# Kernel tuning notes

Measured on AMD Instinct MI355X. Metric: run time of the kernel, lower is better.

## Reference

```python
import jax, jax.numpy as jnp
import numpy as np

B, T, OBS, E, H, A = 256, 128, 512, 1024, 1024, 64


def setup_inputs() -> dict:
    key = jax.random.key(0)
    ks = jax.random.split(key, 8)
    s = 0.02
    return {
        "obs": jax.random.normal(ks[0], (B, T, OBS), jnp.float32),
        "h0": jnp.zeros((B, H), jnp.float32),
        "c0": jnp.zeros((B, H), jnp.float32),
        "W1": jax.random.normal(ks[1], (OBS, E), jnp.float32) * s,
        "b1": jnp.zeros((E,), jnp.float32),
        "W2": jax.random.normal(ks[2], (E, E), jnp.float32) * s,
        "b2": jnp.zeros((E,), jnp.float32),
        "w_ih": jax.random.normal(ks[3], (4 * H, E), jnp.float32) * s,
        "w_hh": jax.random.normal(ks[4], (4 * H, H), jnp.float32) * s,
        "b_ih": jnp.zeros((4 * H,), jnp.float32).at[H:2 * H].set(1.0),  # forget-gate bias init
        "b_hh": jnp.zeros((4 * H,), jnp.float32),
        "ln_g": jnp.ones((H,), jnp.float32),
        "ln_b": jnp.zeros((H,), jnp.float32),
        "Wa": jax.random.normal(ks[5], (H, A), jnp.float32) * s,
        "ba": jnp.zeros((A,), jnp.float32),
        "Wc": jax.random.normal(ks[6], (H, 1), jnp.float32) * s,
        "bc": jnp.zeros((1,), jnp.float32),
        "Wobs": jax.random.normal(ks[7], (H, OBS), jnp.float32) * s,
        "bobs": jnp.zeros((OBS,), jnp.float32),
        "Wr": jax.random.normal(jax.random.fold_in(key, 9), (H, 1), jnp.float32) * s,
        "br": jnp.zeros((1,), jnp.float32),
    }


def _layernorm(x, g, b, eps=1e-5):
    mu = jnp.mean(x, axis=-1, keepdims=True)
    var = jnp.mean(jnp.square(x - mu), axis=-1, keepdims=True)
    return (x - mu) * jax.lax.rsqrt(var + eps) * g + b


def reference(obs, h0, c0, W1, b1, W2, b2, w_ih, w_hh, b_ih, b_hh,
              ln_g, ln_b, Wa, ba, Wc, bc, Wobs, bobs, Wr, br):
    # obs encoder: Linear -> SiLU -> Linear -> SiLU   [B,T,OBS] -> [B,T,E]
    enc = jax.nn.silu(jax.nn.silu(obs @ W1 + b1) @ W2 + b2)
    # precompute input contribution to gates (batched GEMM): [B,T,4H]
    gx = jnp.einsum('bte,ge->btg', enc, w_ih) + (b_ih + b_hh)
    gx_t = jnp.transpose(gx, (1, 0, 2))  # [T,B,4H] for scan

    Hs = h0.shape[-1]

    def step(carry, g_in):
        h, c = carry
        gates = g_in + h @ w_hh.T  # [B,4H]
        i = jax.nn.sigmoid(gates[:, :Hs])
        f = jax.nn.sigmoid(gates[:, Hs:2 * Hs])
        g = jnp.tanh(gates[:, 2 * Hs:3 * Hs])
        o = jax.nn.sigmoid(gates[:, 3 * Hs:])
        new_c = f * c + i * g
        new_h = o * jnp.tanh(new_c)
        return (new_h, new_c), new_h

    (hT, cT), h_seq = jax.lax.scan(step, (h0, c0), gx_t)  # h_seq: [T,B,H]
    h_seq = jnp.transpose(h_seq, (1, 0, 2))  # [B,T,H] batch-first internal format

    x = _layernorm(h_seq, ln_g, ln_b)
    logits = x @ Wa + ba            # [B,T,A]
    values = x @ Wc + bc            # [B,T,1]
    obs_pred = x @ Wobs + bobs      # [B,T,OBS]
    rew_pred = x @ Wr + br          # [B,T,1]
    return (logits, values, obs_pred, rew_pred, hT, cT)
```

## Files before the change

kernel.cpp:

```cpp
#include <hip/hip_runtime.h>
#include <cstdint>

constexpr int Bb = 256, Tt = 128, OBSn = 512, Ee = 1024, Hh = 1024, Aa = 64;
constexpr int Tc = 16;

typedef __attribute__((ext_vector_type(8))) short bf16x8;
typedef __attribute__((ext_vector_type(4))) float floatx4;

__device__ __forceinline__ unsigned short f2bf(float f) {
  union { float f; unsigned u; } c; c.f = f;
  unsigned r = c.u + 0x7fffu + ((c.u >> 16) & 1u);
  return (unsigned short)(r >> 16);
}
__device__ __forceinline__ float bf2f(unsigned short h) {
  union { unsigned u; float f; } c; c.u = ((unsigned)h) << 16; return c.f;
}
__device__ __forceinline__ void gload16(const void* g, void* l) {
  __builtin_amdgcn_global_load_lds(
      (__attribute__((address_space(1))) void*)(uintptr_t)g,
      (__attribute__((address_space(3))) void*)l, 16, 0, 0);
}
__device__ __forceinline__ float sigmoidf_(float x) { return 1.f / (1.f + __expf(-x)); }
__device__ __forceinline__ float tanhf_(float x) { return 2.f / (1.f + __expf(-2.f * x)) - 1.f; }

template <int EPI>
__global__ __launch_bounds__(512) void gemm256(
    const unsigned short* __restrict__ A, const unsigned short* __restrict__ Bt,
    const float* __restrict__ bias, void* __restrict__ Cout,
    int M, int N, int K, int ldo) {
  __shared__ __align__(16) unsigned short sm[4][256 * 64];
  const int tid = threadIdx.x;
  const int wave = tid >> 6, lane = tid & 63;
  const int quad = lane >> 4, l16 = lane & 15;
  const int nwg = gridDim.x;
  const int wg = (blockIdx.x & 7) * (nwg >> 3) + (blockIdx.x >> 3);
  const int nbn = N >> 8;
  const int m0 = (wg / nbn) * 256, n0 = (wg % nbn) * 256;
  const int wm = (wave >> 2) * 128, wn = (wave & 3) * 64;

  floatx4 zero = {0.f, 0.f, 0.f, 0.f};
  floatx4 acc[8][4];
#pragma unroll
  for (int i = 0; i < 8; ++i)
#pragma unroll
    for (int j = 0; j < 4; ++j) acc[i][j] = zero;

  const int nk = K >> 6;
  auto stage = [&](int p, int k0) {
#pragma unroll
    for (int s = 0; s < 4; ++s) {
      const int c = s * 512 + tid;
      const int row = c >> 3;
      const int sl = (c & 7) ^ (row & 7);
      const int lb = (s * 512 + wave * 64) * 8;
      gload16(A + (size_t)(m0 + row) * K + k0 + sl * 8, &sm[p][lb]);
      gload16(Bt + (size_t)(n0 + row) * K + k0 + sl * 8, &sm[2 + p][lb]);
    }
  };
  stage(0, 0);
  stage(1, 1 << 6);
  for (int kt = 0; kt < nk; ++kt) {
    if (kt + 1 < nk) asm volatile("s_waitcnt vmcnt(8)" ::: "memory");
    else             asm volatile("s_waitcnt vmcnt(0)" ::: "memory");
    __builtin_amdgcn_s_barrier();
    const int p = kt & 1;
#pragma unroll
    for (int kk = 0; kk < 2; ++kk) {
      bf16x8 af[8], bfr[4];
#pragma unroll
      for (int i = 0; i < 8; ++i) {
        const int row = wm + i * 16 + l16;
        af[i] = *(const bf16x8*)&sm[p][row * 64 + (((kk * 4 + quad) ^ (l16 & 7)) << 3)];
      }
#pragma unroll
      for (int j = 0; j < 4; ++j) {
        const int row = wn + j * 16 + l16;
        bfr[j] = *(const bf16x8*)&sm[2 + p][row * 64 + (((kk * 4 + quad) ^ (l16 & 7)) << 3)];
      }
#pragma unroll
      for (int i = 0; i < 8; ++i)
#pragma unroll
        for (int j = 0; j < 4; ++j)
          acc[i][j] = __builtin_amdgcn_mfma_f32_16x16x32_bf16(af[i], bfr[j], acc[i][j], 0, 0, 0);
    }
    __builtin_amdgcn_s_barrier();
    if (kt + 2 < nk) stage(p, (kt + 2) << 6);
  }

  if (EPI == 3) {
#pragma unroll
    for (int i = 0; i < 8; ++i)
#pragma unroll
      for (int j = 0; j < 4; ++j) {
        const int col = n0 + wn + j * 16 + l16;
        const float bv = bias[col];
#pragma unroll
        for (int r = 0; r < 4; ++r) {
          const int row = m0 + wm + i * 16 + quad * 4 + r;
          ((float*)Cout)[(size_t)row * ldo + col] = acc[i][j][r] + bv;
        }
      }
  } else {
    __syncthreads();
    unsigned short* Cs = &sm[0][0];
#pragma unroll
    for (int i = 0; i < 8; ++i)
#pragma unroll
      for (int j = 0; j < 4; ++j) {
        const int coll = wn + j * 16 + l16;
        float bv = 0.f;
        if (EPI == 0 || EPI == 1) bv = bias[n0 + coll];
#pragma unroll
        for (int r = 0; r < 4; ++r) {
          const int rowl = wm + i * 16 + quad * 4 + r;
          float v = acc[i][j][r];
          if (EPI == 0 || EPI == 1) {
            v += bv;
            v = v * sigmoidf_(v);
          }
          Cs[rowl * 256 + (coll ^ (quad << 4))] = f2bf(v);
        }
      }
    __syncthreads();
#pragma unroll
    for (int pp = 0; pp < 16; ++pp) {
      const int c2 = pp * 4096 + tid * 8;
      const int rowl = c2 >> 8, coll = c2 & 255;
      const bf16x8 val = *(const bf16x8*)&Cs[rowl * 256 + (coll ^ (((rowl >> 2) & 3) << 4))];
      size_t orow;
      if (EPI == 1) {
        const int grow = m0 + rowl;
        orow = (size_t)((grow & (Tt - 1)) * Bb + (grow >> 7));
      } else {
        orow = (size_t)(m0 + rowl);
      }
      *(bf16x8*)((unsigned short*)Cout + orow * ldo + n0 + coll) = val;
    }
  }
}

template <int EPI>
__global__ __launch_bounds__(256) void gemm_bt(
    const unsigned short* __restrict__ A, const unsigned short* __restrict__ Bt,
    const float* __restrict__ bias, void* __restrict__ Cout,
    int M, int N, int K, int ldo, int nreal) {
  __shared__ __align__(16) unsigned short sm[4][128 * 32];
  const int tid = threadIdx.x;
  const int wave = tid >> 6, lane = tid & 63;
  const int quad = lane >> 4, l16 = lane & 15;
  const int m0 = blockIdx.x * 128, n0 = blockIdx.y * 128;
  const int wm = (wave >> 1) * 64, wn = (wave & 1) * 64;

  floatx4 zero = {0.f, 0.f, 0.f, 0.f};
  floatx4 acc[4][4];
#pragma unroll
  for (int i = 0; i < 4; ++i)
#pragma unroll
    for (int j = 0; j < 4; ++j) acc[i][j] = zero;

  const int nk = K >> 5;
  auto stage = [&](int p, int k0) {
#pragma unroll
    for (int r = 0; r < 2; ++r) {
      const int cb = (r * 4 + wave) * 64;
      const int c = cb + lane;
      const int row = c >> 2, kp = (c & 3) << 3;
      gload16(A + (size_t)(m0 + row) * K + k0 + kp, &sm[p][cb * 8]);
      gload16(Bt + (size_t)(n0 + row) * K + k0 + kp, &sm[2 + p][cb * 8]);
    }
  };
  stage(0, 0);
  for (int kt = 0; kt < nk; ++kt) {
    __syncthreads();
    if (kt + 1 < nk) stage((kt + 1) & 1, (kt + 1) << 5);
    const int p = kt & 1;
    bf16x8 af[4], bfr[4];
#pragma unroll
    for (int i = 0; i < 4; ++i)
      af[i] = *(const bf16x8*)&sm[p][(wm + i * 16 + l16) * 32 + quad * 8];
#pragma unroll
    for (int i = 0; i < 4; ++i)
      bfr[i] = *(const bf16x8*)&sm[2 + p][(wn + i * 16 + l16) * 32 + quad * 8];
#pragma unroll
    for (int i = 0; i < 4; ++i)
#pragma unroll
      for (int j = 0; j < 4; ++j)
        acc[i][j] = __builtin_amdgcn_mfma_f32_16x16x32_bf16(af[i], bfr[j], acc[i][j], 0, 0, 0);
  }
#pragma unroll
  for (int i = 0; i < 4; ++i) {
#pragma unroll
    for (int j = 0; j < 4; ++j) {
      const int col = n0 + wn + j * 16 + l16;
#pragma unroll
      for (int r = 0; r < 4; ++r) {
        const int row = m0 + wm + i * 16 + quad * 4 + r;
        float v = acc[i][j][r];
        if (col < nreal) {
          v += bias[col];
          ((float*)Cout)[(size_t)row * ldo + col] = v;
        }
      }
    }
  }
}

__global__ __launch_bounds__(256) void lstm_step(
    const unsigned short* __restrict__ hprev, long long hstride,
    const unsigned short* __restrict__ whh,
    const unsigned short* __restrict__ gxt,
    const float* __restrict__ bias4h,
    float* __restrict__ c_st, float* __restrict__ hTf,
    unsigned short* __restrict__ hseq_t,
    int write_hT) {
  __shared__ __align__(16) unsigned short As[2][4][64 * 32];
  __shared__ __align__(16) unsigned short Bs[2][4][64 * 32];
  const int bid = blockIdx.x;
  const int xcd = bid & 7, slot = bid >> 3;
  const int m0 = (slot & 3) * 64;
  const int nh0 = (xcd + ((slot >> 2) << 3)) * 16;
  const int tid = threadIdx.x;
  const int wave = tid >> 6, lane = tid & 63;
  const int quad = lane >> 4, l16 = lane & 15;

  floatx4 zero = {0.f, 0.f, 0.f, 0.f};
  floatx4 acc[4] = {zero, zero, zero, zero};

  const int row = tid >> 2, kp = (tid & 3) << 3;
  const int wrow = ((row >> 4) << 10) + nh0 + (row & 15);
  const unsigned short* asrc = hprev + (size_t)(m0 + row) * hstride + kp;
  const unsigned short* bsrc = whh + (size_t)wrow * Hh + kp;

  auto stage = [&](int p, int k0) {
#pragma unroll
    for (int s = 0; s < 4; ++s) {
      gload16(asrc + k0 + s * 32, &As[p][s][wave * 512]);
      gload16(bsrc + k0 + s * 32, &Bs[p][s][wave * 512]);
    }
  };
  stage(0, 0);
  stage(1, 128);
  for (int kt = 0; kt < 8; ++kt) {
    if (kt + 1 < 8) asm volatile("s_waitcnt vmcnt(8)" ::: "memory");
    else            asm volatile("s_waitcnt vmcnt(0)" ::: "memory");
    __builtin_amdgcn_s_barrier();
    const int p = kt & 1;
#pragma unroll
    for (int s = 0; s < 4; ++s) {
      bf16x8 af = *(const bf16x8*)&As[p][s][(wave * 16 + l16) * 32 + quad * 8];
#pragma unroll
      for (int g = 0; g < 4; ++g) {
        bf16x8 bfr = *(const bf16x8*)&Bs[p][s][(g * 16 + l16) * 32 + quad * 8];
        acc[g] = __builtin_amdgcn_mfma_f32_16x16x32_bf16(af, bfr, acc[g], 0, 0, 0);
      }
    }
    __builtin_amdgcn_s_barrier();
    if (kt + 2 < 8) stage(p, (kt + 2) << 7);
  }
  const int col = nh0 + l16;
#pragma unroll
  for (int r = 0; r < 4; ++r) {
    const int b = m0 + wave * 16 + quad * 4 + r;
    float pre[4];
#pragma unroll
    for (int g = 0; g < 4; ++g)
      pre[g] = acc[g][r] + bf2f(gxt[(size_t)b * 4096 + (g << 10) + col]) + bias4h[(g << 10) + col];
    const float ig = sigmoidf_(pre[0]);
    const float fg = sigmoidf_(pre[1]);
    const float gg = tanhf_(pre[2]);
    const float og = sigmoidf_(pre[3]);
    const size_t idx = (size_t)b * Hh + col;
    const float cn = fg * c_st[idx] + ig * gg;
    c_st[idx] = cn;
    const float hn = og * tanhf_(cn);
    if (write_hT) hTf[idx] = hn;
    hseq_t[(size_t)b * (Tt * Hh) + col] = f2bf(hn);
  }
}

__global__ __launch_bounds__(256) void ln_head(
    const unsigned short* __restrict__ hseq, const float* __restrict__ g,
    const float* __restrict__ b, const float* __restrict__ Wc, const float* __restrict__ bc,
    const float* __restrict__ Wr, const float* __restrict__ br,
    unsigned short* __restrict__ xout, float* __restrict__ vout, float* __restrict__ rout) {
  const int row = blockIdx.x;
  const int tid = threadIdx.x;
  const int wave = tid >> 6, lane = tid & 63;
  __shared__ float red[4][4];
  const ushort4 hv = ((const ushort4*)(hseq + (size_t)row * Hh))[tid];
  float h[4] = {bf2f(hv.x), bf2f(hv.y), bf2f(hv.z), bf2f(hv.w)};
  float s = h[0] + h[1] + h[2] + h[3];
  float ss = h[0] * h[0] + h[1] * h[1] + h[2] * h[2] + h[3] * h[3];
#pragma unroll
  for (int o = 32; o > 0; o >>= 1) { s += __shfl_xor(s, o); ss += __shfl_xor(ss, o); }
  if (lane == 0) { red[0][wave] = s; red[1][wave] = ss; }
  __syncthreads();
  s = red[0][0] + red[0][1] + red[0][2] + red[0][3];
  ss = red[1][0] + red[1][1] + red[1][2] + red[1][3];
  const float mu = s * (1.f / 1024.f);
  const float var = ss * (1.f / 1024.f) - mu * mu;
  const float rs = rsqrtf(var + 1e-5f);
  const float4 gv = ((const float4*)g)[tid];
  const float4 bv = ((const float4*)b)[tid];
  const float4 wcv = ((const float4*)Wc)[tid];
  const float4 wrv = ((const float4*)Wr)[tid];
  const float x0 = (h[0] - mu) * rs * gv.x + bv.x;
  const float x1 = (h[1] - mu) * rs * gv.y + bv.y;
  const float x2 = (h[2] - mu) * rs * gv.z + bv.z;
  const float x3 = (h[3] - mu) * rs * gv.w + bv.w;
  ushort4 pk; pk.x = f2bf(x0); pk.y = f2bf(x1); pk.z = f2bf(x2); pk.w = f2bf(x3);
  ((ushort4*)(xout + (size_t)row * Hh))[tid] = pk;
  float v = x0 * wcv.x + x1 * wcv.y + x2 * wcv.z + x3 * wcv.w;
  float r = x0 * wrv.x + x1 * wrv.y + x2 * wrv.z + x3 * wrv.w;
#pragma unroll
  for (int o = 32; o > 0; o >>= 1) { v += __shfl_xor(v, o); r += __shfl_xor(r, o); }
  if (lane == 0) { red[2][wave] = v; red[3][wave] = r; }
  __syncthreads();
  if (tid == 0) {
    vout[row] = red[2][0] + red[2][1] + red[2][2] + red[2][3] + bc[0];
    rout[row] = red[3][0] + red[3][1] + red[3][2] + red[3][3] + br[0];
  }
}

__global__ __launch_bounds__(256) void cvt_bf16x4(const float4* __restrict__ in,
                                                  ushort4* __restrict__ out, int n4) {
  const int i = blockIdx.x * 256 + threadIdx.x;
  if (i < n4) {
    const float4 v = in[i];
    ushort4 o; o.x = f2bf(v.x); o.y = f2bf(v.y); o.z = f2bf(v.z); o.w = f2bf(v.w);
    out[i] = o;
  }
}
__global__ __launch_bounds__(256) void transpose_cvt(const float* __restrict__ in,
                                                     unsigned short* __restrict__ out,
                                                     int K, int N, int NPAD) {
  __shared__ float tile[32][33];
  const int tx = threadIdx.x & 31, ty = threadIdx.x >> 5;
  const int k0 = blockIdx.x * 32, n0 = blockIdx.y * 32;
#pragma unroll
  for (int i = 0; i < 32; i += 8) {
    const int k = k0 + ty + i, n = n0 + tx;
    tile[ty + i][tx] = (n < N && k < K) ? in[(size_t)k * N + n] : 0.f;
  }
  __syncthreads();
#pragma unroll
  for (int i = 0; i < 32; i += 8) {
    const int n = n0 + ty + i, k = k0 + tx;
    if (n < NPAD && k < K) out[(size_t)n * K + k] = f2bf(tile[tx][ty + i]);
  }
}
__global__ __launch_bounds__(256) void prep_kernel(
    const float* __restrict__ b_ih, const float* __restrict__ b_hh, float* __restrict__ bias4h,
    const float* __restrict__ h0, const float* __restrict__ c0,
    unsigned short* __restrict__ h0bf, float* __restrict__ c_st) {
  const int i = blockIdx.x * 256 + threadIdx.x;
  if (i < 4096) bias4h[i] = b_ih[i] + b_hh[i];
  h0bf[i] = f2bf(h0[i]);
  c_st[i] = c0[i];
}
__global__ __launch_bounds__(256) void copy_hc(const float* __restrict__ h,
                                               const float* __restrict__ c,
                                               float* __restrict__ oh, float* __restrict__ oc) {
  const int i = blockIdx.x * 256 + threadIdx.x;
  oh[i] = h[i];
  oc[i] = c[i];
}

constexpr size_t SZ_W1T = (size_t)Ee * OBSn * 2;
constexpr size_t SZ_W2T = (size_t)Ee * Ee * 2;
constexpr size_t SZ_WAT = (size_t)128 * Hh * 2;
constexpr size_t SZ_WOBST = (size_t)OBSn * Hh * 2;
constexpr size_t SZ_WIH = (size_t)4 * Hh * Ee * 2;
constexpr size_t SZ_WHH = (size_t)4 * Hh * Hh * 2;
constexpr size_t SZ_BIAS = 4096 * 4;
constexpr size_t SZ_H0BF = (size_t)Bb * Hh * 2;
constexpr size_t SZ_CST = (size_t)Bb * Hh * 4;
constexpr size_t SZ_HTF = (size_t)Bb * Hh * 4;
constexpr size_t SZ_R1 = (size_t)Bb * Tt * OBSn * 2;
constexpr size_t SZ_R2 = (size_t)Bb * Tt * Ee * 2;

constexpr size_t OFF_W1T = 0;
constexpr size_t OFF_W2T = OFF_W1T + SZ_W1T;
constexpr size_t OFF_WAT = OFF_W2T + SZ_W2T;
constexpr size_t OFF_WOBST = OFF_WAT + SZ_WAT;
constexpr size_t OFF_WIH = OFF_WOBST + SZ_WOBST;
constexpr size_t OFF_WHH = OFF_WIH + SZ_WIH;
constexpr size_t OFF_BIAS = OFF_WHH + SZ_WHH;
constexpr size_t OFF_H0BF = OFF_BIAS + SZ_BIAS;
constexpr size_t OFF_CST = OFF_H0BF + SZ_H0BF;
constexpr size_t OFF_HTF = OFF_CST + SZ_CST;
constexpr size_t OFF_R1 = OFF_HTF + SZ_HTF;
constexpr size_t OFF_R2 = OFF_R1 + SZ_R1;
constexpr size_t WS_NEED = OFF_R2 + SZ_R2;

constexpr size_t OFF_LOGITS = 0;
constexpr size_t OFF_V = (size_t)Bb * Tt * Aa;
constexpr size_t OFF_OBS = OFF_V + (size_t)Bb * Tt;
constexpr size_t OFF_R = OFF_OBS + (size_t)Bb * Tt * OBSn;
constexpr size_t OFF_HT = OFF_R + (size_t)Bb * Tt;
constexpr size_t OFF_CT = OFF_HT + (size_t)Bb * Hh;

extern "C" void kernel_launch(void* const* d_in, const int* in_sizes, int n_in,
                              void* d_out, int out_size, void* d_ws, size_t ws_size,
                              hipStream_t stream) {
  if (ws_size < WS_NEED) return;

  const float* obs = (const float*)d_in[0];
  const float* h0 = (const float*)d_in[1];
  const float* c0 = (const float*)d_in[2];
  const float* W1 = (const float*)d_in[3];
  const float* b1 = (const float*)d_in[4];
  const float* W2 = (const float*)d_in[5];
  const float* b2 = (const float*)d_in[6];
  const float* w_ih = (const float*)d_in[7];
  const float* w_hh = (const float*)d_in[8];
  const float* b_ih = (const float*)d_in[9];
  const float* b_hh = (const float*)d_in[10];
  const float* ln_g = (const float*)d_in[11];
  const float* ln_b = (const float*)d_in[12];
  const float* Wa = (const float*)d_in[13];
  const float* ba = (const float*)d_in[14];
  const float* Wc = (const float*)d_in[15];
  const float* bc = (const float*)d_in[16];
  const float* Wobs = (const float*)d_in[17];
  const float* bobs = (const float*)d_in[18];
  const float* Wr = (const float*)d_in[19];
  const float* br = (const float*)d_in[20];

  char* ws = (char*)d_ws;
  unsigned short* w1t = (unsigned short*)(ws + OFF_W1T);
  unsigned short* w2t = (unsigned short*)(ws + OFF_W2T);
  unsigned short* wat = (unsigned short*)(ws + OFF_WAT);
  unsigned short* wobst = (unsigned short*)(ws + OFF_WOBST);
  unsigned short* wih = (unsigned short*)(ws + OFF_WIH);
  unsigned short* whh = (unsigned short*)(ws + OFF_WHH);
  float* bias4h = (float*)(ws + OFF_BIAS);
  unsigned short* h0bf = (unsigned short*)(ws + OFF_H0BF);
  float* cst = (float*)(ws + OFF_CST);
  float* htf = (float*)(ws + OFF_HTF);
  unsigned short* obsbf = (unsigned short*)(ws + OFF_R1);
  unsigned short* gxc = (unsigned short*)(ws + OFF_R1);
  unsigned short* enc2t = (unsigned short*)(ws + OFF_R2);
  unsigned short* xbuf = (unsigned short*)(ws + OFF_R2);
  float* out = (float*)d_out;
  unsigned short* enc1 = (unsigned short*)(out + OFF_OBS);
  unsigned short* hseq = (unsigned short*)(out + OFF_OBS);

  const dim3 blk(256);
  const dim3 blk512(512);

  prep_kernel<<<dim3(1024), blk, 0, stream>>>(b_ih, b_hh, bias4h, h0, c0, h0bf, cst);
  cvt_bf16x4<<<dim3(16384), blk, 0, stream>>>((const float4*)obs, (ushort4*)obsbf, 4194304);
  cvt_bf16x4<<<dim3(4096), blk, 0, stream>>>((const float4*)w_ih, (ushort4*)wih, 1048576);
  cvt_bf16x4<<<dim3(4096), blk, 0, stream>>>((const float4*)w_hh, (ushort4*)whh, 1048576);
  transpose_cvt<<<dim3(16, 32), blk, 0, stream>>>(W1, w1t, OBSn, Ee, Ee);
  transpose_cvt<<<dim3(32, 32), blk, 0, stream>>>(W2, w2t, Ee, Ee, Ee);
  transpose_cvt<<<dim3(32, 4), blk, 0, stream>>>(Wa, wat, Hh, Aa, 128);
  transpose_cvt<<<dim3(32, 16), blk, 0, stream>>>(Wobs, wobst, Hh, OBSn, OBSn);

  gemm256<0><<<dim3(512), blk512, 0, stream>>>(obsbf, w1t, b1, enc1, 32768, Ee, OBSn, Ee);
  gemm256<1><<<dim3(512), blk512, 0, stream>>>(enc1, w2t, b2, enc2t, 32768, Ee, Ee, Ee);

  for (int ch = 0; ch < Tt / Tc; ++ch) {
    gemm256<2><<<dim3(256), blk512, 0, stream>>>(enc2t + (size_t)ch * Tc * Bb * Ee, wih, nullptr,
                                                 gxc, Tc * Bb, 4096, Ee, 4096);
    for (int l = 0; l < Tc; ++l) {
      const int t = ch * Tc + l;
      const unsigned short* hp = (t == 0) ? h0bf : hseq + (size_t)(t - 1) * Hh;
      const long long hs = (t == 0) ? (long long)Hh : (long long)Tt * Hh;
      lstm_step<<<dim3(256), blk, 0, stream>>>(hp, hs, whh, gxc + (size_t)l * Bb * 4096,
                                               bias4h, cst, htf, hseq + (size_t)t * Hh,
                                               (t == Tt - 1) ? 1 : 0);
    }
  }

  ln_head<<<dim3(32768), blk, 0, stream>>>(hseq, ln_g, ln_b, Wc, bc, Wr, br, xbuf,
                                           out + OFF_V, out + OFF_R);
  gemm_bt<3><<<dim3(256, 1), blk, 0, stream>>>(xbuf, wat, ba, out + OFF_LOGITS, 32768, 128, Hh, Aa, Aa);
  gemm256<3><<<dim3(256), blk512, 0, stream>>>(xbuf, wobst, bobs, out + OFF_OBS, 32768, OBSn, Hh, OBSn);
  copy_hc<<<dim3(1024), blk, 0, stream>>>(htf, cst, out + OFF_HT, out + OFF_CT);

  (void)in_sizes; (void)n_in; (void)out_size;
}
```

Before: 2.031 ms.

## Interleave GEMM tile prefetch chunks with MFMA quarter-steps and raise wave priority

```diff
diff --git a/kernel.cpp b/kernel.cpp
--- a/kernel.cpp
+++ b/kernel.cpp
@@ -22,6 +22,11 @@
 }
 __device__ __forceinline__ float sigmoidf_(float x) { return 1.f / (1.f + __expf(-x)); }
 __device__ __forceinline__ float tanhf_(float x) { return 2.f / (1.f + __expf(-2.f * x)) - 1.f; }
+
+template <int N> __device__ __forceinline__ void waitv() {
+  if constexpr (N == 0) asm volatile("s_waitcnt vmcnt(0)" ::: "memory");
+  else asm volatile("s_waitcnt vmcnt(2)" ::: "memory");
+}
 
 template <int EPI>
 __global__ __launch_bounds__(512) void gemm256(
@@ -46,45 +51,58 @@
     for (int j = 0; j < 4; ++j) acc[i][j] = zero;
 
   const int nk = K >> 6;
-  auto stage = [&](int p, int k0) {
-#pragma unroll
-    for (int s = 0; s < 4; ++s) {
-      const int c = s * 512 + tid;
-      const int row = c >> 3;
-      const int sl = (c & 7) ^ (row & 7);
-      const int lb = (s * 512 + wave * 64) * 8;
-      gload16(A + (size_t)(m0 + row) * K + k0 + sl * 8, &sm[p][lb]);
-      gload16(Bt + (size_t)(n0 + row) * K + k0 + sl * 8, &sm[2 + p][lb]);
-    }
+  auto sub = [&](const unsigned short* G, int gb, int r0, int k0, unsigned short* dst) {
+    const int row = r0 + (tid >> 3);
+    const int sl = (tid & 7) ^ (row & 7);
+    gload16(G + (size_t)(gb + row) * K + k0 + sl * 8, dst + (size_t)(r0 * 8 + wave * 64) * 8);
   };
-  stage(0, 0);
-  stage(1, 1 << 6);
-  for (int kt = 0; kt < nk; ++kt) {
-    if (kt + 1 < nk) asm volatile("s_waitcnt vmcnt(8)" ::: "memory");
-    else             asm volatile("s_waitcnt vmcnt(0)" ::: "memory");
-    __builtin_amdgcn_s_barrier();
-    const int p = kt & 1;
-#pragma unroll
-    for (int kk = 0; kk < 2; ++kk) {
-      bf16x8 af[8], bfr[4];
-#pragma unroll
-      for (int i = 0; i < 8; ++i) {
-        const int row = wm + i * 16 + l16;
-        af[i] = *(const bf16x8*)&sm[p][row * 64 + (((kk * 4 + quad) ^ (l16 & 7)) << 3)];
-      }
-#pragma unroll
-      for (int j = 0; j < 4; ++j) {
-        const int row = wn + j * 16 + l16;
-        bfr[j] = *(const bf16x8*)&sm[2 + p][row * 64 + (((kk * 4 + quad) ^ (l16 & 7)) << 3)];
-      }
-#pragma unroll
-      for (int i = 0; i < 8; ++i)
+  auto stagec = [&](int c, int k0, unsigned short* dA, unsigned short* dB) {
+    if (c == 0)      { sub(A, m0, 0, k0, dA);    sub(Bt, n0, 0, k0, dB); }
+    else if (c == 1) { sub(A, m0, 128, k0, dA);  sub(Bt, n0, 64, k0, dB); }
+    else if (c == 2) { sub(Bt, n0, 128, k0, dB); sub(Bt, n0, 192, k0, dB); }
+    else             { sub(A, m0, 64, k0, dA);   sub(A, m0, 192, k0, dA); }
+  };
+
+#pragma unroll
+  for (int c = 0; c < 4; ++c) stagec(c, 0, &sm[0][0], &sm[2][0]);
+
+  for (int T = 0; T < nk; ++T) {
+    const int e = T & 1;
+    const unsigned short* sA = &sm[e][0];
+    const unsigned short* sB = &sm[2 + e][0];
+    unsigned short* dA = &sm[e ^ 1][0];
+    unsigned short* dB = &sm[2 + (e ^ 1)][0];
+    const bool lastT = (T + 1 == nk);
+    bf16x8 bfr[4];
+#pragma unroll
+    for (int q = 0; q < 4; ++q) {
+      if (q == 0) waitv<2>();
+      else if (q == 1) {
+        if (lastT) waitv<0>(); else waitv<2>();
+      }
+      asm volatile("s_barrier" ::: "memory");
+      const int kk = q >> 1, ihi = (q & 1) * 4, ro = (q & 1) * 64;
+      bf16x8 af[4];
+#pragma unroll
+      for (int i = 0; i < 4; ++i)
+        af[i] = *(const bf16x8*)&sA[(wm + ro + i * 16 + l16) * 64 +
+                                    (((kk * 4 + quad) ^ (l16 & 7)) << 3)];
+      if ((q & 1) == 0) {
 #pragma unroll
         for (int j = 0; j < 4; ++j)
-          acc[i][j] = __builtin_amdgcn_mfma_f32_16x16x32_bf16(af[i], bfr[j], acc[i][j], 0, 0, 0);
-    }
-    __builtin_amdgcn_s_barrier();
-    if (kt + 2 < nk) stage(p, (kt + 2) << 6);
+          bfr[j] = *(const bf16x8*)&sB[(wn + j * 16 + l16) * 64 +
+                                       (((kk * 4 + quad) ^ (l16 & 7)) << 3)];
+      }
+      if (!lastT) stagec(q, (T + 1) << 6, dA, dB);
+      __builtin_amdgcn_s_setprio(1);
+#pragma unroll
+      for (int i = 0; i < 4; ++i)
+#pragma unroll
+        for (int j = 0; j < 4; ++j)
+          acc[ihi + i][j] =
+              __builtin_amdgcn_mfma_f32_16x16x32_bf16(af[i], bfr[j], acc[ihi + i][j], 0, 0, 0);
+      __builtin_amdgcn_s_setprio(0);
+    }
   }
 
   if (EPI == 3) {
```

After: 2.035 ms. Within noise of the previous version (+0.2%).
